# Kernel optimization log

Hardware: AMD Instinct MI355X
Metric: run time of the kernel (lower is better)

Reference implementation:

```python
import jax, jax.numpy as jnp
import numpy as np

ACT = jax.nn.relu
REG = 1.0  # semi_dual_sgd passes reg=1 (not self.e)
N_ITER = 1000


def _convt(x, w, b, out_pad):
    # PyTorch ConvTranspose2d, w layout [Cin, Cout, kh, kw], k=3, stride=2, padding=1
    wk = jnp.transpose(w[:, :, ::-1, ::-1], (1, 0, 2, 3))  # -> OIHW
    y = jax.lax.conv_general_dilated(
        x, wk, window_strides=(1, 1),
        padding=((1, 1 + out_pad), (1, 1 + out_pad)),
        lhs_dilation=(2, 2),
        dimension_numbers=("NCHW", "OIHW", "NCHW"))
    return y + b[None, :, None, None]


def _conv(x, w, b):
    # Conv2d k=3, padding=1, w layout OIHW
    y = jax.lax.conv_general_dilated(
        x, w, window_strides=(1, 1), padding=((1, 1), (1, 1)),
        dimension_numbers=("NCHW", "OIHW", "NCHW"))
    return y + b[None, :, None, None]


def _decoder_logits(z, fc_w, fc_b, ct0_w, ct0_b, ct1_w, ct1_b, fct_w, fct_b, conv_w, conv_b):
    h = ACT(z @ fc_w + fc_b)            # [n, 128*16]
    h = h.reshape(-1, 128, 4, 4)
    h = ACT(_convt(h, ct0_w, ct0_b, 0))  # [n, 64, 7, 7]  (img_size==28 branch: output_padding=0)
    h = ACT(_convt(h, ct1_w, ct1_b, 1))  # [n, 32, 14, 14]
    h = ACT(_convt(h, fct_w, fct_b, 1))  # [n, 32, 28, 28]
    return _conv(h, conv_w, conv_b)      # [n, 1, 28, 28] Bernoulli logits


def _cost_matrix(x, logit):
    # C[i,j] = -sum_pix Bernoulli(logits=logit_j).log_prob(x_i)
    # log_prob = x*logit - softplus(logit); sum over pixels factorizes into a GEMM.
    B = x.shape[0]
    n = logit.shape[0]
    X = x.reshape(B, -1)          # [B, P]
    L = logit.reshape(n, -1)      # [n, P]
    sp = jnp.sum(jax.nn.softplus(L), axis=1)  # [n]
    return -(X @ L.T) + sp[None, :]           # [B, n]


def _sag_semi_dual(C, idx, reg):
    # SAG on the semi-dual entropic OT objective (Genevay et al. / POT-style),
    # uniform marginals, lr = reg / max(a) = reg * n_src.
    n_src, n_tgt = C.shape
    a = jnp.full((n_src,), 1.0 / n_src, dtype=C.dtype)
    b = jnp.full((n_tgt,), 1.0 / n_tgt, dtype=C.dtype)
    log_b = jnp.log(b)
    lr = reg * n_src

    def step(carry, i):
        beta, stored, ssum = carry
        # stable softmax form of exp(-(C[i]-beta)/reg)*b / sum(...)
        khi = jax.nn.softmax((beta - C[i]) / reg + log_b)
        g = a[i] * (b - khi)
        ssum = ssum + g - stored[i]
        stored = stored.at[i].set(g)
        beta = beta + (lr / n_src) * ssum
        return (beta, stored, ssum), None

    init = (jnp.zeros((n_tgt,), C.dtype), jnp.zeros((n_src, n_tgt), C.dtype), jnp.zeros((n_tgt,), C.dtype))
    (beta, _, _), _ = jax.lax.scan(step, init, idx)

    # entropic c-transform and primal plan recovery
    alpha = -reg * jax.scipy.special.logsumexp((beta[None, :] - C) / reg + log_b[None, :], axis=1)
    P = jnp.exp((alpha[:, None] + beta[None, :] - C) / reg) * a[:, None] * b[None, :]
    return P, a, b


def _omega(x):
    xs = jnp.where(x <= 0.0, 1.0, x)
    return jnp.sum(xs * jnp.log(xs))


def setup_inputs() -> dict:
    key = jax.random.key(0)
    ks = jax.random.split(key, 16)
    B, N, LAT = 512, 512, 64
    s = 0.05
    return {
        "x": jax.random.uniform(ks[0], (B, 1, 28, 28), jnp.float32),
        "z": jax.random.normal(ks[1], (N, LAT), jnp.float32),
        "fc_w": jax.random.normal(ks[2], (LAT, 128 * 16), jnp.float32) * s,
        "fc_b": jnp.zeros((128 * 16,), jnp.float32),
        "ct0_w": jax.random.normal(ks[3], (128, 64, 3, 3), jnp.float32) * s,
        "ct0_b": jnp.zeros((64,), jnp.float32),
        "ct1_w": jax.random.normal(ks[4], (64, 32, 3, 3), jnp.float32) * s,
        "ct1_b": jnp.zeros((32,), jnp.float32),
        "fct_w": jax.random.normal(ks[5], (32, 32, 3, 3), jnp.float32) * s,
        "fct_b": jnp.zeros((32,), jnp.float32),
        "conv_w": jax.random.normal(ks[6], (1, 32, 3, 3), jnp.float32) * s,
        "conv_b": jnp.zeros((1,), jnp.float32),
        "idx": jax.random.randint(ks[7], (N_ITER,), 0, B, jnp.int32),
    }


def reference(x, z, fc_w, fc_b, ct0_w, ct0_b, ct1_w, ct1_b, fct_w, fct_b, conv_w, conv_b, idx):
    logit = _decoder_logits(z, fc_w, fc_b, ct0_w, ct0_b, ct1_w, ct1_b, fct_w, fct_b, conv_w, conv_b)
    C = _cost_matrix(x, logit)                 # [B, n_sample]
    P, px, pz = _sag_semi_dual(C, idx, REG)    # numItermax=1000, reg=1
    kl = _omega(P) - _omega(px) - _omega(pz)
    return (P, C, kl)
```

## Files before the change

kernel.cpp:

```cpp
#include <hip/hip_runtime.h>
#include <hip/hip_bf16.h>
#include <math.h>


typedef float vf4 __attribute__((ext_vector_type(4)));

#define RFL(v) __builtin_amdgcn_readfirstlane(v)

__global__ void fc_relu_k(const float* __restrict__ z, const float* __restrict__ w,
                          const float* __restrict__ b, float* __restrict__ out) {
  int n = blockIdx.x >> 1;
  int c0 = ((blockIdx.x & 1) << 10) + threadIdx.x * 4;
  const float* zr = z + n * 64;
  float4 acc = *(const float4*)&b[c0];
#pragma unroll
  for (int k = 0; k < 64; ++k) {
    float zk = zr[k];
    float4 wv = *(const float4*)&w[k * 2048 + c0];
    acc.x = fmaf(zk, wv.x, acc.x);
    acc.y = fmaf(zk, wv.y, acc.y);
    acc.z = fmaf(zk, wv.z, acc.z);
    acc.w = fmaf(zk, wv.w, acc.w);
  }
  acc.x = fmaxf(acc.x, 0.f); acc.y = fmaxf(acc.y, 0.f);
  acc.z = fmaxf(acc.z, 0.f); acc.w = fmaxf(acc.w, 0.f);
  *(float4*)&out[n * 2048 + c0] = acc;
}

template <int CIN, int COUT, int HIN, int HOUT, int GW>
__global__ void convt_pair_k(const float* __restrict__ x, const float* __restrict__ w,
                             const float* __restrict__ bias, float* __restrict__ y) {
  constexpr bool FULL = (HOUT == 2 * HIN);
  constexpr int QP = HIN * HIN;
  __shared__ float wt[9 * CIN * GW];
  const int tid = threadIdx.x;
  const int g0 = blockIdx.y * GW;
  for (int e = tid; e < 9 * CIN * GW; e += 256) {
    int cl = e % GW;
    int rest = e / GW;
    int ci = rest & (CIN - 1);
    int t = rest / CIN;
    wt[e] = w[((size_t)ci * COUT + g0 + cl) * 9 + t];
  }
  __syncthreads();

  int q = blockIdx.x * 256 + tid;
  int np = q / QP;
  int pq = q % QP;
  int a = pq / HIN, b = pq % HIN;
  const bool oka = (a + 1 < HIN), okb = (b + 1 < HIN);
  const float* xim0 = x + (size_t)np * CIN * QP + a * HIN + b;
  const float* xim1 = x + (size_t)(np + 256) * CIN * QP + a * HIN + b;

  float acc0[4][GW], acc1[4][GW];
#pragma unroll
  for (int p = 0; p < 4; ++p)
#pragma unroll
    for (int c = 0; c < GW; ++c) { acc0[p][c] = 0.f; acc1[p][c] = 0.f; }

#define TAPW(T, P, XV0, XV1) { \
  if constexpr (GW == 4) { \
    float4 wv_ = *reinterpret_cast<const float4*>(&wt[((T) * CIN + ci) * 4]); \
    acc0[P][0] = fmaf(XV0, wv_.x, acc0[P][0]); \
    acc0[P][1] = fmaf(XV0, wv_.y, acc0[P][1]); \
    acc0[P][2] = fmaf(XV0, wv_.z, acc0[P][2]); \
    acc0[P][3] = fmaf(XV0, wv_.w, acc0[P][3]); \
    acc1[P][0] = fmaf(XV1, wv_.x, acc1[P][0]); \
    acc1[P][1] = fmaf(XV1, wv_.y, acc1[P][1]); \
    acc1[P][2] = fmaf(XV1, wv_.z, acc1[P][2]); \
    acc1[P][3] = fmaf(XV1, wv_.w, acc1[P][3]); \
  } else { \
    float2 wv_ = *reinterpret_cast<const float2*>(&wt[((T) * CIN + ci) * 2]); \
    acc0[P][0] = fmaf(XV0, wv_.x, acc0[P][0]); \
    acc0[P][1] = fmaf(XV0, wv_.y, acc0[P][1]); \
    acc1[P][0] = fmaf(XV1, wv_.x, acc1[P][0]); \
    acc1[P][1] = fmaf(XV1, wv_.y, acc1[P][1]); \
  } }

  for (int ci = 0; ci < CIN; ++ci) {
    const float* xc0 = xim0 + ci * QP;
    const float* xc1 = xim1 + ci * QP;
    float p00 = xc0[0];
    float p01 = okb ? xc0[1] : 0.f;
    float p10 = oka ? xc0[HIN] : 0.f;
    float p11 = (oka && okb) ? xc0[HIN + 1] : 0.f;
    float q00 = xc1[0];
    float q01 = okb ? xc1[1] : 0.f;
    float q10 = oka ? xc1[HIN] : 0.f;
    float q11 = (oka && okb) ? xc1[HIN + 1] : 0.f;
    TAPW(4, 0, p00, q00)
    TAPW(3, 1, p01, q01) TAPW(5, 1, p00, q00)
    TAPW(1, 2, p10, q10) TAPW(7, 2, p00, q00)
    TAPW(0, 3, p11, q11) TAPW(2, 3, p10, q10) TAPW(6, 3, p01, q01) TAPW(8, 3, p00, q00)
  }
#undef TAPW

  int oh0 = 2 * a, ow0 = 2 * b;
  bool vh = FULL || (oh0 + 1 < HOUT);
  bool vw = FULL || (ow0 + 1 < HOUT);
#pragma unroll
  for (int c = 0; c < GW; ++c) {
    float bv = bias[g0 + c];
    float a00 = fmaxf(acc0[0][c] + bv, 0.f);
    float a01 = fmaxf(acc0[1][c] + bv, 0.f);
    float a10 = fmaxf(acc0[2][c] + bv, 0.f);
    float a11 = fmaxf(acc0[3][c] + bv, 0.f);
    float b00 = fmaxf(acc1[0][c] + bv, 0.f);
    float b01 = fmaxf(acc1[1][c] + bv, 0.f);
    float b10 = fmaxf(acc1[2][c] + bv, 0.f);
    float b11 = fmaxf(acc1[3][c] + bv, 0.f);
    float* yb0 = y + (((size_t)np * COUT + g0 + c) * HOUT + oh0) * (size_t)HOUT + ow0;
    float* yb1 = y + (((size_t)(np + 256) * COUT + g0 + c) * HOUT + oh0) * (size_t)HOUT + ow0;
    if (FULL) {
      *(float2*)yb0 = make_float2(a00, a01);
      *(float2*)(yb0 + HOUT) = make_float2(a10, a11);
      *(float2*)yb1 = make_float2(b00, b01);
      *(float2*)(yb1 + HOUT) = make_float2(b10, b11);
    } else {
      yb0[0] = a00;
      yb1[0] = b00;
      if (vw) { yb0[1] = a01; yb1[1] = b01; }
      if (vh) { yb0[HOUT] = a10; yb1[HOUT] = b10; }
      if (vh && vw) { yb0[HOUT + 1] = a11; yb1[HOUT + 1] = b11; }
    }
  }
}

__global__ void conv_final_pair_k(const float* __restrict__ x, const float* __restrict__ w,
                                  const float* __restrict__ bias, float* __restrict__ y) {
  __shared__ float ws_[288];
  int tid = threadIdx.x;
  if (tid < 288) ws_[tid] = w[tid];
  __syncthreads();
  int gid = blockIdx.x * 256 + tid;
  int px = gid % 784;
  int np = gid / 784;
  int ow = px % 28;
  int oh = px / 28;
  bool h0 = oh > 0, h2 = oh < 27, w0 = ow > 0, w2 = ow < 27;
  const float* xb0 = x + (size_t)np * 32 * 784 + (oh - 1) * 28 + (ow - 1);
  const float* xb1 = x + (size_t)(np + 256) * 32 * 784 + (oh - 1) * 28 + (ow - 1);
  float acc0 = bias[0], acc1 = bias[0];
  for (int ci = 0; ci < 32; ++ci) {
    const float* xc0 = xb0 + ci * 784;
    const float* xc1 = xb1 + ci * 784;
    const float* wc = &ws_[ci * 9];
    if (h0 && w0) { acc0 = fmaf(xc0[0], wc[0], acc0); acc1 = fmaf(xc1[0], wc[0], acc1); }
    if (h0)       { acc0 = fmaf(xc0[1], wc[1], acc0); acc1 = fmaf(xc1[1], wc[1], acc1); }
    if (h0 && w2) { acc0 = fmaf(xc0[2], wc[2], acc0); acc1 = fmaf(xc1[2], wc[2], acc1); }
    if (w0)       { acc0 = fmaf(xc0[28], wc[3], acc0); acc1 = fmaf(xc1[28], wc[3], acc1); }
                    acc0 = fmaf(xc0[29], wc[4], acc0); acc1 = fmaf(xc1[29], wc[4], acc1);
    if (w2)       { acc0 = fmaf(xc0[30], wc[5], acc0); acc1 = fmaf(xc1[30], wc[5], acc1); }
    if (h2 && w0) { acc0 = fmaf(xc0[56], wc[6], acc0); acc1 = fmaf(xc1[56], wc[6], acc1); }
    if (h2)       { acc0 = fmaf(xc0[57], wc[7], acc0); acc1 = fmaf(xc1[57], wc[7], acc1); }
    if (h2 && w2) { acc0 = fmaf(xc0[58], wc[8], acc0); acc1 = fmaf(xc1[58], wc[8], acc1); }
  }
  y[(size_t)np * 784 + px] = acc0;
  y[(size_t)(np + 256) * 784 + px] = acc1;
}

template <int CTRL>
__device__ __forceinline__ float dpp_f(float x) {
  return __int_as_float(__builtin_amdgcn_update_dpp(0, __float_as_int(x), CTRL, 0xF, 0xF, true));
}
__device__ __forceinline__ float rdl(float v, int l) {
  return __int_as_float(__builtin_amdgcn_readlane(__float_as_int(v), l));
}
__device__ __forceinline__ float wsum64_l63(float v) {
  v += dpp_f<0xB1>(v);
  v += dpp_f<0x4E>(v);
  v += dpp_f<0x141>(v);
  v += dpp_f<0x140>(v);
  v += dpp_f<0x142>(v);
  v += dpp_f<0x143>(v);
  return rdl(v, 63);
}
__device__ __forceinline__ float wmax64_l63(float v) {
  v = fmaxf(v, dpp_f<0xB1>(v));
  v = fmaxf(v, dpp_f<0x4E>(v));
  v = fmaxf(v, dpp_f<0x141>(v));
  v = fmaxf(v, dpp_f<0x140>(v));
  v = fmaxf(v, dpp_f<0x142>(v));
  v = fmaxf(v, dpp_f<0x143>(v));
  return rdl(v, 63);
}

__global__ void cost_k(const float* __restrict__ X, const float* __restrict__ L,
                       float* __restrict__ Craw, float* __restrict__ sp) {
  __shared__ float Xs[16][20];
  __shared__ float Ls[16][68];
  int tid = threadIdx.x;
  int i0 = blockIdx.y * 16, j0 = blockIdx.x * 64;
  int lrow = tid >> 2;
  int lq = tid & 3;
  int xrow = tid & 15;
  int xq = (tid >> 4) & 3;
  bool doX = tid < 64;
  bool doSP = (blockIdx.y == 0);
  int tx = tid & 15, ty = tid >> 4;
  float acc[4] = {};
  float spacc = 0.f;
  for (int k0 = 0; k0 < 784; k0 += 16) {
    float4 lv = *(const float4*)&L[(size_t)(j0 + lrow) * 784 + k0 + lq * 4];
    float4 xv = {0.f, 0.f, 0.f, 0.f};
    if (doX) xv = *(const float4*)&X[(size_t)(i0 + xrow) * 784 + k0 + xq * 4];
    __syncthreads();
    Ls[lq * 4 + 0][lrow] = lv.x; Ls[lq * 4 + 1][lrow] = lv.y;
    Ls[lq * 4 + 2][lrow] = lv.z; Ls[lq * 4 + 3][lrow] = lv.w;
    if (doX) {
      Xs[xq * 4 + 0][xrow] = xv.x; Xs[xq * 4 + 1][xrow] = xv.y;
      Xs[xq * 4 + 2][xrow] = xv.z; Xs[xq * 4 + 3][xrow] = xv.w;
    }
    if (doSP) {
      spacc += fmaxf(lv.x, 0.f) + log1pf(__expf(-fabsf(lv.x)));
      spacc += fmaxf(lv.y, 0.f) + log1pf(__expf(-fabsf(lv.y)));
      spacc += fmaxf(lv.z, 0.f) + log1pf(__expf(-fabsf(lv.z)));
      spacc += fmaxf(lv.w, 0.f) + log1pf(__expf(-fabsf(lv.w)));
    }
    __syncthreads();
#pragma unroll
    for (int k = 0; k < 16; ++k) {
      float a = Xs[k][ty];
      float4 bq = *(const float4*)&Ls[k][tx * 4];
      acc[0] = fmaf(a, bq.x, acc[0]); acc[1] = fmaf(a, bq.y, acc[1]);
      acc[2] = fmaf(a, bq.z, acc[2]); acc[3] = fmaf(a, bq.w, acc[3]);
    }
  }
  float4 o = make_float4(acc[0], acc[1], acc[2], acc[3]);
  *(float4*)&Craw[(size_t)(i0 + ty) * 512 + j0 + tx * 4] = o;
  if (doSP) {
    float q = spacc;
    q += dpp_f<0xB1>(q);
    q += dpp_f<0x4E>(q);
    if (lq == 0) sp[j0 + lrow] = q;
  }
}

__global__ void prep_k(const float* __restrict__ craw, const float* __restrict__ sp,
                       float* __restrict__ D2, float* __restrict__ stored,
                       float* __restrict__ klout) {
  __shared__ float part[4];
  int i = blockIdx.x, tid = threadIdx.x;
  int wid = tid >> 6, lane = tid & 63;
  stored[(size_t)i * 512 + tid] = 0.f;
  stored[(size_t)i * 512 + tid + 256] = 0.f;
  if (i == 0 && tid == 0) klout[0] = 12.476649250079016f;
  float c0 = craw[(size_t)i * 512 + tid];
  float c1 = craw[(size_t)i * 512 + tid + 256];
  float v0 = c0 - sp[tid];
  float v1 = c1 - sp[tid + 256];
  float wm = wmax64_l63(fmaxf(v0, v1));
  if (lane == 0) part[wid] = wm;
  __syncthreads();
  float m = fmaxf(fmaxf(part[0], part[1]), fmaxf(part[2], part[3]));
  const float L2E = 1.4426950408889634f;
  D2[(size_t)i * 512 + tid] = (m - v0) * L2E;
  D2[(size_t)i * 512 + tid + 256] = (m - v1) * L2E;
}

#define SLD0(ROW) { const float* cp_ = D2 + ((size_t)(unsigned)(ROW) << 9) + jb; \
  s0dA = *(const vf4*)cp_; s0dB = *(const vf4*)(cp_ + 4); \
  const float* tp_ = stored + ((size_t)(unsigned)(ROW) << 9) + jb; \
  s0sA = *(const vf4*)tp_; s0sB = *(const vf4*)(tp_ + 4); }
#define SLD1(ROW) { const float* cp_ = D2 + ((size_t)(unsigned)(ROW) << 9) + jb; \
  s1dA = *(const vf4*)cp_; s1dB = *(const vf4*)(cp_ + 4); \
  const float* tp_ = stored + ((size_t)(unsigned)(ROW) << 9) + jb; \
  s1sA = *(const vf4*)tp_; s1sB = *(const vf4*)(tp_ + 4); }

#define STEP(RR, PFR, DA, DB, SA, SB, LDM, \
             R1,A1,B1, R2,A2,B2, R3,A3,B3, R4,A4,B4, R5,A5,B5, R6,A6,B6, \
             GA, GB) \
{ \
  vf4 d0_ = DA, d1_ = DB, t0_ = SA, t1_ = SB; \
  LDM(PFR); \
  const int r_ = (RR); \
  if (__builtin_expect((r_==(R1)) | (r_==(R2)) | (r_==(R3)) | \
                       (r_==(R4)) | (r_==(R5)) | (r_==(R6)), 0)) { \
    if (r_==(R6)) { t0_ = A6; t1_ = B6; } \
    if (r_==(R5)) { t0_ = A5; t1_ = B5; } \
    if (r_==(R4)) { t0_ = A4; t1_ = B4; } \
    if (r_==(R3)) { t0_ = A3; t1_ = B3; } \
    if (r_==(R2)) { t0_ = A2; t1_ = B2; } \
    if (r_==(R1)) { t0_ = A1; t1_ = B1; } \
  } \
  vf4 u0_ = ssumL - t0_; \
  vf4 u1_ = ssumH - t1_; \
  vf4 a0_ = betaL - d0_; \
  vf4 a1_ = betaH - d1_; \
  vf4 e0_, e1_; \
  e0_.x = __builtin_amdgcn_exp2f(a0_.x); e0_.y = __builtin_amdgcn_exp2f(a0_.y); \
  e0_.z = __builtin_amdgcn_exp2f(a0_.z); e0_.w = __builtin_amdgcn_exp2f(a0_.w); \
  e1_.x = __builtin_amdgcn_exp2f(a1_.x); e1_.y = __builtin_amdgcn_exp2f(a1_.y); \
  e1_.z = __builtin_amdgcn_exp2f(a1_.z); e1_.w = __builtin_amdgcn_exp2f(a1_.w); \
  vf4 es_ = e0_ + e1_; \
  float S_ = wsum64_l63((es_.x + es_.z) + (es_.y + es_.w)); \
  S_ = fmaxf(S_, 1e-35f); \
  float kk_ = C2NL * __builtin_amdgcn_rcpf(S_); \
  vf4 g0_ = e0_ * kk_ + c1l4; \
  vf4 g1_ = e1_ * kk_ + c1l4; \
  ssumL = u0_ + g0_; ssumH = u1_ + g1_; \
  betaL += ssumL; betaH += ssumH; \
  float* wp_ = stored + ((size_t)(unsigned)r_ << 9) + jb; \
  *(vf4*)wp_ = g0_; *(vf4*)(wp_ + 4) = g1_; \
  GA = g0_; GB = g1_; \
}

__global__ void __launch_bounds__(512, 1) sag_k(const float* __restrict__ D2,
                                                const int* __restrict__ idx,
                                                float* __restrict__ stored,
                                                float* __restrict__ beta_out) {
  const int tid = threadIdx.x;
  if (tid >= 64) {
    const vf4* c4 = (const vf4*)D2;
    const vf4* s4 = (const vf4*)stored;
    vf4 acc = {0.f, 0.f, 0.f, 0.f};
    for (int p = tid - 64; p < 65536; p += 448) { acc += c4[p]; acc += s4[p]; }
    float accs = acc.x + acc.y + acc.z + acc.w;
    asm volatile("" :: "v"(accs));
    return;
  }

  const int jb = tid * 8;
  const float C2NL = -0.0028177637f;
  const vf4 c1l4 = {5.503574e-06f, 5.503574e-06f, 5.503574e-06f, 5.503574e-06f};

  vf4 z4 = {0.f, 0.f, 0.f, 0.f};
  vf4 betaL = z4, betaH = z4, ssumL = z4, ssumH = z4;
  vf4 h1A = z4, h1B = z4, h2A = z4, h2B = z4, h3A = z4, h3B = z4;
  vf4 h4A = z4, h4B = z4, h5A = z4, h5B = z4, h6A = z4, h6B = z4;
  int hr1 = -1, hr2 = -1, hr3 = -1, hr4 = -1, hr5 = -1, hr6 = -1;
  float vsh = 0.f;

  int i0 = RFL(idx[0]), i1 = RFL(idx[1]), i2 = RFL(idx[2]), i3 = RFL(idx[3]);
  int i4 = RFL(idx[4]), i5 = RFL(idx[5]), i6 = RFL(idx[6]), i7 = RFL(idx[7]);

  vf4 s0dA, s0dB, s0sA, s0sB, s1dA, s1dB, s1sA, s1sB;
  SLD0(i0);
  SLD1(i1);

  vf4 g0a, g0b, g1a, g1b, g2a, g2b, g3a, g3b;
  vf4 g4a, g4b, g5a, g5b, g6a, g6b, g7a, g7b;

  for (int t = 0; t < 1000; t += 8) {
    int tb = (t + 8 < 1000) ? (t + 8) : 992;
    int n0 = RFL(idx[tb + 0]), n1 = RFL(idx[tb + 1]);
    int n2 = RFL(idx[tb + 2]), n3 = RFL(idx[tb + 3]);
    int n4 = RFL(idx[tb + 4]), n5 = RFL(idx[tb + 5]);
    int n6 = RFL(idx[tb + 6]), n7 = RFL(idx[tb + 7]);

    STEP(i0, i2, s0dA, s0dB, s0sA, s0sB, SLD0,
         hr1,h1A,h1B, hr2,h2A,h2B, hr3,h3A,h3B, hr4,h4A,h4B, hr5,h5A,h5B, hr6,h6A,h6B,
         g0a, g0b)
    STEP(i1, i3, s1dA, s1dB, s1sA, s1sB, SLD1,
         i0,g0a,g0b, hr1,h1A,h1B, hr2,h2A,h2B, hr3,h3A,h3B, hr4,h4A,h4B, hr5,h5A,h5B,
         g1a, g1b)
    STEP(i2, i4, s0dA, s0dB, s0sA, s0sB, SLD0,
         i1,g1a,g1b, i0,g0a,g0b, hr1,h1A,h1B, hr2,h2A,h2B, hr3,h3A,h3B, hr4,h4A,h4B,
         g2a, g2b)
    STEP(i3, i5, s1dA, s1dB, s1sA, s1sB, SLD1,
         i2,g2a,g2b, i1,g1a,g1b, i0,g0a,g0b, hr1,h1A,h1B, hr2,h2A,h2B, hr3,h3A,h3B,
         g3a, g3b)
    STEP(i4, i6, s0dA, s0dB, s0sA, s0sB, SLD0,
         i3,g3a,g3b, i2,g2a,g2b, i1,g1a,g1b, i0,g0a,g0b, hr1,h1A,h1B, hr2,h2A,h2B,
         g4a, g4b)
    STEP(i5, i7, s1dA, s1dB, s1sA, s1sB, SLD1,
         i4,g4a,g4b, i3,g3a,g3b, i2,g2a,g2b, i1,g1a,g1b, i0,g0a,g0b, hr1,h1A,h1B,
         g5a, g5b)
    STEP(i6, n0, s0dA, s0dB, s0sA, s0sB, SLD0,
         i5,g5a,g5b, i4,g4a,g4b, i3,g3a,g3b, i2,g2a,g2b, i1,g1a,g1b, i0,g0a,g0b,
         g6a, g6b)
    STEP(i7, n1, s1dA, s1dB, s1sA, s1sB, SLD1,
         i6,g6a,g6b, i5,g5a,g5b, i4,g4a,g4b, i3,g3a,g3b, i2,g2a,g2b, i1,g1a,g1b,
         g7a, g7b)

    {
      vf4 qm;
      qm.x = fmaxf(betaL.x, betaH.x); qm.y = fmaxf(betaL.y, betaH.y);
      qm.z = fmaxf(betaL.z, betaH.z); qm.w = fmaxf(betaL.w, betaH.w);
      float lm = fmaxf(fmaxf(qm.x, qm.y), fmaxf(qm.z, qm.w));
      float dm = wmax64_l63(lm);
      betaL = betaL - dm; betaH = betaH - dm;
      vsh += dm;
    }

    hr1 = i7; h1A = g7a; h1B = g7b;
    hr2 = i6; h2A = g6a; h2B = g6b;
    hr3 = i5; h3A = g5a; h3B = g5b;
    hr4 = i4; h4A = g4a; h4B = g4b;
    hr5 = i3; h5A = g3a; h5B = g3b;
    hr6 = i2; h6A = g2a; h6B = g2b;
    i0 = n0; i1 = n1; i2 = n2; i3 = n3;
    i4 = n4; i5 = n5; i6 = n6; i7 = n7;
  }

  const float LN2 = 0.6931471805599453f;
  vf4 oL = (betaL + vsh) * LN2;
  vf4 oH = (betaH + vsh) * LN2;
  *(vf4*)(beta_out + jb) = oL;
  *(vf4*)(beta_out + jb + 4) = oH;
}

__global__ void p_k(const float* __restrict__ craw, const float* __restrict__ sp,
                    const float* __restrict__ beta, float* __restrict__ P,
                    float* __restrict__ Cout, float* __restrict__ klout) {
  __shared__ float part[12];
  int i = blockIdx.x, tid = threadIdx.x;
  int wid = tid >> 6, lane = tid & 63;
  float c0 = craw[(size_t)i * 512 + tid];
  float c1 = craw[(size_t)i * 512 + tid + 256];
  float sp0 = sp[tid], sp1 = sp[tid + 256];
  float u0 = (beta[tid] - sp0) + c0;
  float u1 = (beta[tid + 256] - sp1) + c1;
  Cout[(size_t)i * 512 + tid] = sp0 - c0;
  Cout[(size_t)i * 512 + tid + 256] = sp1 - c1;
  float wm = wmax64_l63(fmaxf(u0, u1));
  if (lane == 0) part[wid] = wm;
  __syncthreads();
  float m = fmaxf(fmaxf(part[0], part[1]), fmaxf(part[2], part[3]));
  float e0 = __expf(u0 - m), e1 = __expf(u1 - m);
  float ws = wsum64_l63(e0 + e1);
  if (lane == 0) part[4 + wid] = ws;
  __syncthreads();
  float S = (part[4] + part[5]) + (part[6] + part[7]);
  float lse = m + logf(S);
  const float log512 = 6.238324625039508f;
  float p0 = __expf(u0 - lse) * (1.0f / 512.0f);
  float p1 = __expf(u1 - lse) * (1.0f / 512.0f);
  P[(size_t)i * 512 + tid] = p0;
  P[(size_t)i * 512 + tid + 256] = p1;
  float pl = p0 * (u0 - lse - log512) + p1 * (u1 - lse - log512);
  float wp = wsum64_l63(pl);
  if (lane == 0) part[8 + wid] = wp;
  __syncthreads();
  if (tid == 0)
    atomicAdd(klout, (part[8] + part[9]) + (part[10] + part[11]));
}

extern "C" void kernel_launch(void* const* d_in, const int* in_sizes, int n_in,
                              void* d_out, int out_size, void* d_ws, size_t ws_size,
                              hipStream_t stream) {
  const float* x = (const float*)d_in[0];
  const float* z = (const float*)d_in[1];
  const float* fc_w = (const float*)d_in[2];
  const float* fc_b = (const float*)d_in[3];
  const float* ct0_w = (const float*)d_in[4];
  const float* ct0_b = (const float*)d_in[5];
  const float* ct1_w = (const float*)d_in[6];
  const float* ct1_b = (const float*)d_in[7];
  const float* fct_w = (const float*)d_in[8];
  const float* fct_b = (const float*)d_in[9];
  const float* conv_w = (const float*)d_in[10];
  const float* conv_b = (const float*)d_in[11];
  const int* idx = (const int*)d_in[12];

  float* out = (float*)d_out;
  float* Pout = out;
  float* Cout = out + 262144;
  float* klout = out + 524288;

  float* ws = (float*)d_ws;
  float* h0 = ws;
  float* h1 = h0 + 1048576;
  float* h2 = h1 + 1605632;
  float* h3 = h2 + 3211264;
  float* logit = h3 + 12845056;
  float* sp = logit + 401408;
  float* beta = sp + 512;
  float* stored = beta + 512;
  float* Craw = h0;
  float* D2 = h1;

  fc_relu_k<<<1024, 256, 0, stream>>>(z, fc_w, fc_b, h0);
  convt_pair_k<128, 64, 4, 7, 2><<<dim3(16, 32), 256, 0, stream>>>(h0, ct0_w, ct0_b, h1);
  convt_pair_k<64, 32, 7, 14, 2><<<dim3(49, 16), 256, 0, stream>>>(h1, ct1_w, ct1_b, h2);
  convt_pair_k<32, 32, 14, 28, 4><<<dim3(196, 8), 256, 0, stream>>>(h2, fct_w, fct_b, h3);
  conv_final_pair_k<<<784, 256, 0, stream>>>(h3, conv_w, conv_b, logit);
  cost_k<<<dim3(8, 32), 256, 0, stream>>>(x, logit, Craw, sp);
  prep_k<<<512, 256, 0, stream>>>(Craw, sp, D2, stored, klout);
  sag_k<<<1, 512, 0, stream>>>(D2, idx, stored, beta);
  p_k<<<512, 256, 0, stream>>>(Craw, sp, beta, Pout, Cout, klout);
}
```

Baseline: 506.7 us.

## Fuse prep, SAG scan and P computation into one persistent kernel with grid sync

The separate prep, single-block SAG and P kernels are merged into one 513-block launch. Block 0 spins until all 512 row blocks have written D2 and zeroed stored, then runs the sequential SAG scan and sets a flag. The other blocks wait on that flag and then compute P, C and KL. This removes two kernel launch boundaries, but it adds a memset launch and relies on all 513 blocks being co-resident, otherwise the spin-waits could deadlock.

```diff
diff --git a/kernel.cpp b/kernel.cpp
--- a/kernel.cpp
+++ b/kernel.cpp
@@ -234,28 +234,6 @@
     q += dpp_f<0x4E>(q);
     if (lq == 0) sp[j0 + lrow] = q;
   }
-}
-
-__global__ void prep_k(const float* __restrict__ craw, const float* __restrict__ sp,
-                       float* __restrict__ D2, float* __restrict__ stored,
-                       float* __restrict__ klout) {
-  __shared__ float part[4];
-  int i = blockIdx.x, tid = threadIdx.x;
-  int wid = tid >> 6, lane = tid & 63;
-  stored[(size_t)i * 512 + tid] = 0.f;
-  stored[(size_t)i * 512 + tid + 256] = 0.f;
-  if (i == 0 && tid == 0) klout[0] = 12.476649250079016f;
-  float c0 = craw[(size_t)i * 512 + tid];
-  float c1 = craw[(size_t)i * 512 + tid + 256];
-  float v0 = c0 - sp[tid];
-  float v1 = c1 - sp[tid + 256];
-  float wm = wmax64_l63(fmaxf(v0, v1));
-  if (lane == 0) part[wid] = wm;
-  __syncthreads();
-  float m = fmaxf(fmaxf(part[0], part[1]), fmaxf(part[2], part[3]));
-  const float L2E = 1.4426950408889634f;
-  D2[(size_t)i * 512 + tid] = (m - v0) * L2E;
-  D2[(size_t)i * 512 + tid + 256] = (m - v1) * L2E;
 }
 
 #define SLD0(ROW) { const float* cp_ = D2 + ((size_t)(unsigned)(ROW) << 9) + jb; \
@@ -305,11 +283,8 @@
   GA = g0_; GB = g1_; \
 }
 
-__global__ void __launch_bounds__(512, 1) sag_k(const float* __restrict__ D2,
-                                                const int* __restrict__ idx,
-                                                float* __restrict__ stored,
-                                                float* __restrict__ beta_out) {
-  const int tid = threadIdx.x;
+__device__ void sag_scan(const float* __restrict__ D2, const int* __restrict__ idx,
+                         float* __restrict__ stored, float* __restrict__ beta_out, int tid) {
   if (tid >= 64) {
     const vf4* c4 = (const vf4*)D2;
     const vf4* s4 = (const vf4*)stored;
@@ -400,40 +375,85 @@
   *(vf4*)(beta_out + jb + 4) = oH;
 }
 
-__global__ void p_k(const float* __restrict__ craw, const float* __restrict__ sp,
-                    const float* __restrict__ beta, float* __restrict__ P,
-                    float* __restrict__ Cout, float* __restrict__ klout) {
-  __shared__ float part[12];
-  int i = blockIdx.x, tid = threadIdx.x;
-  int wid = tid >> 6, lane = tid & 63;
-  float c0 = craw[(size_t)i * 512 + tid];
-  float c1 = craw[(size_t)i * 512 + tid + 256];
-  float sp0 = sp[tid], sp1 = sp[tid + 256];
-  float u0 = (beta[tid] - sp0) + c0;
-  float u1 = (beta[tid + 256] - sp1) + c1;
-  Cout[(size_t)i * 512 + tid] = sp0 - c0;
-  Cout[(size_t)i * 512 + tid + 256] = sp1 - c1;
-  float wm = wmax64_l63(fmaxf(u0, u1));
+__global__ __launch_bounds__(512, 6) void sagfused_k(
+    const float* __restrict__ craw, const float* __restrict__ sp,
+    const int* __restrict__ idx,
+    float* __restrict__ D2, float* __restrict__ stored, float* __restrict__ beta,
+    float* __restrict__ Pout, float* __restrict__ Cout, float* __restrict__ klout,
+    unsigned* __restrict__ sync) {
+  __shared__ float part[24];
+  const int bid = blockIdx.x;
+  const int tid = threadIdx.x;
+  const int wid = tid >> 6, lane = tid & 63;
+  unsigned* cnt = sync;
+  unsigned* flag = sync + 32;
+
+  if (bid == 0) {
+    if (tid == 0) {
+      while (__hip_atomic_load(cnt, __ATOMIC_RELAXED, __HIP_MEMORY_SCOPE_AGENT) < 512u)
+        __builtin_amdgcn_s_sleep(8);
+      __threadfence();
+      klout[0] = 12.476649250079016f;
+    }
+    __syncthreads();
+    sag_scan(D2, idx, stored, beta, tid);
+    __syncthreads();
+    if (tid == 0) {
+      __threadfence();
+      __hip_atomic_store(flag, 1u, __ATOMIC_RELEASE, __HIP_MEMORY_SCOPE_AGENT);
+    }
+    return;
+  }
+
+  const int i = bid - 1;
+  stored[(size_t)i * 512 + tid] = 0.f;
+  float c = craw[(size_t)i * 512 + tid];
+  float spv = sp[tid];
+  float v = c - spv;
+  float wm = wmax64_l63(v);
   if (lane == 0) part[wid] = wm;
   __syncthreads();
-  float m = fmaxf(fmaxf(part[0], part[1]), fmaxf(part[2], part[3]));
-  float e0 = __expf(u0 - m), e1 = __expf(u1 - m);
-  float ws = wsum64_l63(e0 + e1);
-  if (lane == 0) part[4 + wid] = ws;
-  __syncthreads();
-  float S = (part[4] + part[5]) + (part[6] + part[7]);
+  float m8 = fmaxf(fmaxf(fmaxf(part[0], part[1]), fmaxf(part[2], part[3])),
+                   fmaxf(fmaxf(part[4], part[5]), fmaxf(part[6], part[7])));
+  const float L2E = 1.4426950408889634f;
+  D2[(size_t)i * 512 + tid] = (m8 - v) * L2E;
+  __syncthreads();
+  if (tid == 0) {
+    __threadfence();
+    __hip_atomic_fetch_add(cnt, 1u, __ATOMIC_RELAXED, __HIP_MEMORY_SCOPE_AGENT);
+  }
+  Cout[(size_t)i * 512 + tid] = spv - c;
+  if (tid == 0) {
+    while (__hip_atomic_load(flag, __ATOMIC_RELAXED, __HIP_MEMORY_SCOPE_AGENT) == 0u)
+      __builtin_amdgcn_s_sleep(32);
+    __threadfence();
+  }
+  __syncthreads();
+  float u = (beta[tid] - spv) + c;
+  float wmx = wmax64_l63(u);
+  if (lane == 0) part[wid] = wmx;
+  __syncthreads();
+  float m = fmaxf(fmaxf(fmaxf(part[0], part[1]), fmaxf(part[2], part[3])),
+                  fmaxf(fmaxf(part[4], part[5]), fmaxf(part[6], part[7])));
+  float e = __expf(u - m);
+  float wsm = wsum64_l63(e);
+  if (lane == 0) part[8 + wid] = wsm;
+  __syncthreads();
+  float S = ((part[8] + part[9]) + (part[10] + part[11])) +
+            ((part[12] + part[13]) + (part[14] + part[15]));
   float lse = m + logf(S);
   const float log512 = 6.238324625039508f;
-  float p0 = __expf(u0 - lse) * (1.0f / 512.0f);
-  float p1 = __expf(u1 - lse) * (1.0f / 512.0f);
-  P[(size_t)i * 512 + tid] = p0;
-  P[(size_t)i * 512 + tid + 256] = p1;
-  float pl = p0 * (u0 - lse - log512) + p1 * (u1 - lse - log512);
+  float p = __expf(u - lse) * (1.0f / 512.0f);
+  Pout[(size_t)i * 512 + tid] = p;
+  float pl = p * (u - lse - log512);
   float wp = wsum64_l63(pl);
-  if (lane == 0) part[8 + wid] = wp;
-  __syncthreads();
-  if (tid == 0)
-    atomicAdd(klout, (part[8] + part[9]) + (part[10] + part[11]));
+  if (lane == 0) part[16 + wid] = wp;
+  __syncthreads();
+  if (tid == 0) {
+    float rs = ((part[16] + part[17]) + (part[18] + part[19])) +
+               ((part[20] + part[21]) + (part[22] + part[23]));
+    atomicAdd(klout, rs);
+  }
 }
 
 extern "C" void kernel_launch(void* const* d_in, const int* in_sizes, int n_in,
@@ -467,8 +487,11 @@
   float* sp = logit + 401408;
   float* beta = sp + 512;
   float* stored = beta + 512;
+  unsigned* sync = (unsigned*)(stored + 262144);
   float* Craw = h0;
   float* D2 = h1;
+
+  hipMemsetAsync(sync, 0, 64 * sizeof(unsigned), stream);
 
   fc_relu_k<<<1024, 256, 0, stream>>>(z, fc_w, fc_b, h0);
   convt_pair_k<128, 64, 4, 7, 2><<<dim3(16, 32), 256, 0, stream>>>(h0, ct0_w, ct0_b, h1);
@@ -476,7 +499,6 @@
   convt_pair_k<32, 32, 14, 28, 4><<<dim3(196, 8), 256, 0, stream>>>(h2, fct_w, fct_b, h3);
   conv_final_pair_k<<<784, 256, 0, stream>>>(h3, conv_w, conv_b, logit);
   cost_k<<<dim3(8, 32), 256, 0, stream>>>(x, logit, Craw, sp);
-  prep_k<<<512, 256, 0, stream>>>(Craw, sp, D2, stored, klout);
-  sag_k<<<1, 512, 0, stream>>>(D2, idx, stored, beta);
-  p_k<<<512, 256, 0, stream>>>(Craw, sp, beta, Pout, Cout, klout);
-}
+  sagfused_k<<<513, 512, 0, stream>>>(Craw, sp, idx, D2, stored, beta,
+                                      Pout, Cout, klout, sync);
+}
```

New measurement: 917.7 us (median of 3 runs). +81.1%, slower.
